# Kernel optimization log

Hardware: AMD Instinct MI355X
Metric: run time of the kernel (lower is better)

Reference implementation:

```python
import jax, jax.numpy as jnp
import numpy as np

EPS = 1e-6


def setup_inputs() -> dict:
    key = jax.random.key(0)
    k = jax.random.split(key, 6)
    B, C_in, C_out, H, W, E = 32, 256, 256, 64, 64, 1024
    x = jax.random.normal(k[0], (B, C_in, H, W), dtype=jnp.float32)
    emb = jax.random.normal(k[1], (B, E), dtype=jnp.float32)
    # adaLN Linear(E -> 2*C_in). (Module zero-inits these; random here for coverage.)
    ada_w = jax.random.normal(k[2], (2 * C_in, E), dtype=jnp.float32) * 0.02
    ada_b = jax.random.normal(k[3], (2 * C_in,), dtype=jnp.float32) * 0.02
    # 1x1 Conv2d(C_in -> C_out) weight (C_out, C_in) and bias
    conv_w = jax.random.normal(k[4], (C_out, C_in), dtype=jnp.float32) * (1.0 / np.sqrt(C_in))
    conv_b = jax.random.normal(k[5], (C_out,), dtype=jnp.float32) * 0.02
    return {"x": x, "emb": emb, "ada_w": ada_w, "ada_b": ada_b,
            "conv_w": conv_w, "conv_b": conv_b}


def reference(x, emb, ada_w, ada_b, conv_w, conv_b):
    # adaLN modulation: SiLU(emb) @ W^T + b -> (B, 2C) -> shift, scale
    mod = jax.nn.silu(emb) @ ada_w.T + ada_b          # (B, 2C)
    shift, scale = jnp.split(mod, 2, axis=1)          # each (B, C)
    # RMSNorm over channel dim (no affine)
    rms = jax.lax.rsqrt(jnp.mean(x * x, axis=1, keepdims=True) + EPS)  # (B,1,H,W)
    xn = x * rms
    # modulate: x * (1 + scale) + shift, broadcast over H,W
    xm = xn * (1.0 + scale[:, :, None, None]) + shift[:, :, None, None]
    # 1x1 conv == channel GEMM
    y = jnp.einsum('bchw,oc->bohw', xm, conv_w) + conv_b[None, :, None, None]
    return jax.nn.selu(y)
```

## Files before the change

### kernel.cpp

```cpp
#include <hip/hip_runtime.h>
#include <hip/hip_bf16.h>

typedef __attribute__((ext_vector_type(4))) float f32x4;
typedef __attribute__((ext_vector_type(8))) short s16x8;
typedef __attribute__((ext_vector_type(4))) unsigned short u16x4;

__device__ __forceinline__ unsigned short f2bf(float f) {
  unsigned u = __builtin_bit_cast(unsigned, f);
  u += 0x7fffu + ((u >> 16) & 1u);
  return (unsigned short)(u >> 16);
}

__global__ __launch_bounds__(512) void k_mod(const float* __restrict__ emb,
                                             const float* __restrict__ ada_w,
                                             const float* __restrict__ ada_b,
                                             float* __restrict__ mod) {
  __shared__ __align__(16) float semb[32][1028];
  const int t = threadIdx.x;
  for (int i = t; i < 8192; i += 512) {
    f32x4 v = ((const f32x4*)emb)[i];
    f32x4 s;
#pragma unroll
    for (int j = 0; j < 4; ++j) s[j] = v[j] / (1.f + __expf(-v[j]));
    *(f32x4*)&semb[i >> 8][(i & 255) << 2] = s;
  }
  __syncthreads();
  const int jl = t >> 5, b = t & 31;
  const int j = blockIdx.x * 16 + jl;
  const f32x4* aw = (const f32x4*)(ada_w + (size_t)j * 1024);
  float acc = 0.f;
  for (int q = 0; q < 256; ++q) {
    f32x4 a = aw[q];
    f32x4 sv = *(const f32x4*)&semb[b][q * 4];
    acc += a[0] * sv[0] + a[1] * sv[1] + a[2] * sv[2] + a[3] * sv[3];
  }
  mod[b * 512 + j] = acc + ada_b[j];
}

__global__ __launch_bounds__(256) void k_prep(const float* __restrict__ mod,
                                              const float* __restrict__ conv_w,
                                              const float* __restrict__ conv_b,
                                              unsigned short* __restrict__ wp,
                                              float* __restrict__ dvec) {
  const int b = blockIdx.y;
  const int o = blockIdx.x * 4 + (threadIdx.x >> 6);
  const int l = threadIdx.x & 63;
  const float* sh = mod + b * 512;
  const float* sc = mod + b * 512 + 256;
  f32x4 cw = ((const f32x4*)(conv_w + (size_t)o * 256))[l];
  f32x4 s4 = ((const f32x4*)sc)[l];
  f32x4 h4 = ((const f32x4*)sh)[l];
  u16x4 wq;
#pragma unroll
  for (int j = 0; j < 4; ++j) wq[j] = f2bf(cw[j] * (1.f + s4[j]));
  const int wr = o >> 6, m = (o >> 4) & 3, lr = o & 15;
  const int kk = l >> 3, g = (l >> 1) & 3, jb = 4 * (l & 1);
  *(u16x4*)(wp + (size_t)b * 65536 + (((wr * 4 + m) * 8 + kk) * 512 + g * 128 + lr * 8 + jb)) = wq;
  float dd = cw[0] * h4[0] + cw[1] * h4[1] + cw[2] * h4[2] + cw[3] * h4[3];
#pragma unroll
  for (int off = 32; off; off >>= 1) dd += __shfl_down(dd, off);
  if (l == 0) dvec[b * 256 + o] = dd + conv_b[o];
}

__global__ __launch_bounds__(512, 2) void k_main(const float* __restrict__ x,
                                                 const unsigned short* __restrict__ wp,
                                                 const float* __restrict__ dvec,
                                                 float* __restrict__ out) {
  constexpr int HW = 4096;
  __shared__ __align__(16) float xf[2][32][256];
  __shared__ float prt[2][256];
  __shared__ float rms[256];

  const int t = threadIdx.x;
  const int b = blockIdx.y;
  const int s0 = blockIdx.x * 256;
  const int w = t >> 6, lane = t & 63;
  const int wr = w >> 1, wc = w & 1;
  const int lr = lane & 15, g = lane >> 4;

  const float* xb = x + (size_t)b * (256 * HW) + s0;
  const unsigned short* A2 = wp + (size_t)b * 65536;

#define ISSUE(K, BUF)                                                                     \
  {                                                                                       \
    _Pragma("unroll") for (int i = 0; i < 4; ++i) {                                       \
      const float* gp = xb + (size_t)((K)*32 + w * 4 + i) * HW + lane * 4;                \
      void* lp = (void*)&xf[BUF][w * 4 + i][0];                                           \
      __builtin_amdgcn_global_load_lds((const __attribute__((address_space(1))) void*)gp, \
                                       (__attribute__((address_space(3))) void*)lp, 16,   \
                                       0, 0);                                             \
    }                                                                                     \
  }

  ISSUE(0, 0);
  ISSUE(1, 1);

  const int sS = t & 255, ch = t >> 8;
  float rs = 0.f;
  f32x4 acc[4][8];
#pragma unroll
  for (int m = 0; m < 4; ++m)
#pragma unroll
    for (int n = 0; n < 8; ++n) acc[m][n] = f32x4{0.f, 0.f, 0.f, 0.f};

#pragma unroll
  for (int k = 0; k < 8; ++k) {
    const int buf = k & 1;
    if (k < 7) {
      asm volatile("s_waitcnt vmcnt(4)" ::: "memory");
    } else {
      asm volatile("s_waitcnt vmcnt(0)" ::: "memory");
    }
    __builtin_amdgcn_s_barrier();

#pragma unroll
    for (int i = 0; i < 16; ++i) {
      float v = xf[buf][ch * 16 + i][sS];
      rs += v * v;
    }

    s16x8 af[4];
#pragma unroll
    for (int m = 0; m < 4; ++m)
      af[m] = *(const s16x8*)(A2 + (((wr * 4 + m) * 8 + k) * 512 + lane * 8));
#pragma unroll
    for (int n = 0; n < 8; ++n) {
      const int s = 128 * wc + 16 * n + lr;
      s16x8 bf;
#pragma unroll
      for (int j = 0; j < 8; ++j) bf[j] = (short)f2bf(xf[buf][g * 8 + j][s]);
#pragma unroll
      for (int m = 0; m < 4; ++m)
        acc[m][n] = __builtin_amdgcn_mfma_f32_16x16x32_bf16(af[m], bf, acc[m][n], 0, 0, 0);
    }

    asm volatile("s_waitcnt lgkmcnt(0)" ::: "memory");
    __builtin_amdgcn_s_barrier();
    if (k < 6) ISSUE(k + 2, buf);
  }
#undef ISSUE

  prt[ch][sS] = rs;
  __syncthreads();
  if (t < 256) rms[t] = rsqrtf((prt[0][t] + prt[1][t]) * (1.0f / 256.0f) + 1e-6f);
  __syncthreads();

  float rr[8];
#pragma unroll
  for (int n = 0; n < 8; ++n) rr[n] = rms[128 * wc + 16 * n + lr];
  float* ob = out + (size_t)b * (256 * HW) + s0;
#pragma unroll
  for (int m = 0; m < 4; ++m) {
    const int o0 = 64 * wr + 16 * m + 4 * g;
    const f32x4 dv = *(const f32x4*)(dvec + (size_t)b * 256 + o0);
#pragma unroll
    for (int n = 0; n < 8; ++n) {
#pragma unroll
      for (int r = 0; r < 4; ++r) {
        float v = rr[n] * acc[m][n][r] + dv[r];
        float res = v > 0.f ? 1.0507009873554805f * v
                            : 1.7580993408473766f * (__expf(v) - 1.f);
        ob[(size_t)(o0 + r) * HW + 128 * wc + 16 * n + lr] = res;
      }
    }
  }
}

extern "C" void kernel_launch(void* const* d_in, const int* in_sizes, int n_in,
                              void* d_out, int out_size, void* d_ws, size_t ws_size,
                              hipStream_t stream) {
  const float* x      = (const float*)d_in[0];
  const float* emb    = (const float*)d_in[1];
  const float* ada_w  = (const float*)d_in[2];
  const float* ada_b  = (const float*)d_in[3];
  const float* conv_w = (const float*)d_in[4];
  const float* conv_b = (const float*)d_in[5];
  float* out = (float*)d_out;

  float* mod  = (float*)d_ws;
  float* dvec = mod + 32 * 512;
  unsigned short* wp = (unsigned short*)(dvec + 32 * 256);

  k_mod<<<dim3(32), 512, 0, stream>>>(emb, ada_w, ada_b, mod);
  k_prep<<<dim3(64, 32), 256, 0, stream>>>(mod, conv_w, conv_b, wp, dvec);
  k_main<<<dim3(16, 32), 512, 0, stream>>>(x, wp, dvec, out);
}
```

Baseline: 102.8 us.

## Convert x tile to bf16 once per block into swizzled LDS buffer

Each k-step now has all threads read the fp32 x tile once with vector loads. They accumulate the sum of squares and write a transposed, XOR-swizzled bf16 copy into a separate LDS region. The MFMA B-fragments are then fetched with a single 16-byte LDS read each. Before, every wave did eight strided scalar reads plus bf16 conversions per fragment, repeated across the four row-waves. The RMS reduction moves to cross-lane shuffles. The cost is an extra barrier per k-step and more LDS (80KB per block), which could limit occupancy.

Result: faster. 98.85 us (-3.9%).

```diff
diff --git a/kernel.cpp b/kernel.cpp
--- a/kernel.cpp
+++ b/kernel.cpp
@@ -67,9 +67,11 @@
                                                  const float* __restrict__ dvec,
                                                  float* __restrict__ out) {
   constexpr int HW = 4096;
-  __shared__ __align__(16) float xf[2][32][256];
-  __shared__ float prt[2][256];
-  __shared__ float rms[256];
+  __shared__ __align__(16) unsigned char smem[81920];
+  float(*xf)[32][256] = (float(*)[32][256])smem;
+  unsigned char* bt = smem + 65536;
+  float* prt = (float*)(smem + 65536);
+  float* rms = (float*)(smem + 65536 + 1024);
 
   const int t = threadIdx.x;
   const int b = blockIdx.y;
@@ -95,8 +97,10 @@
   ISSUE(0, 0);
   ISSUE(1, 1);
 
-  const int sS = t & 255, ch = t >> 8;
-  float rs = 0.f;
+  const int cg = lane >> 3;
+  const int sl = 8 * w + (lane & 7);
+  f32x4 ssq = {0.f, 0.f, 0.f, 0.f};
+
   f32x4 acc[4][8];
 #pragma unroll
   for (int m = 0; m < 4; ++m)
@@ -111,13 +115,23 @@
     } else {
       asm volatile("s_waitcnt vmcnt(0)" ::: "memory");
     }
+    asm volatile("s_waitcnt lgkmcnt(0)" ::: "memory");
     __builtin_amdgcn_s_barrier();
 
-#pragma unroll
-    for (int i = 0; i < 16; ++i) {
-      float v = xf[buf][ch * 16 + i][sS];
-      rs += v * v;
-    }
+    f32x4 vv[4];
+#pragma unroll
+    for (int dc = 0; dc < 4; ++dc) vv[dc] = *(const f32x4*)&xf[buf][4 * cg + dc][4 * sl];
+#pragma unroll
+    for (int dc = 0; dc < 4; ++dc) ssq += vv[dc] * vv[dc];
+#pragma unroll
+    for (int si = 0; si < 4; ++si) {
+      const int s = 4 * sl + si;
+      const int vs = (s >> 4) & 3;
+      u16x4 pk = {f2bf(vv[0][si]), f2bf(vv[1][si]), f2bf(vv[2][si]), f2bf(vv[3][si])};
+      *(u16x4*)(bt + s * 64 + ((cg ^ (2 * vs)) << 3)) = pk;
+    }
+    asm volatile("s_waitcnt lgkmcnt(0)" ::: "memory");
+    __builtin_amdgcn_s_barrier();
 
     s16x8 af[4];
 #pragma unroll
@@ -126,23 +140,26 @@
 #pragma unroll
     for (int n = 0; n < 8; ++n) {
       const int s = 128 * wc + 16 * n + lr;
-      s16x8 bf;
-#pragma unroll
-      for (int j = 0; j < 8; ++j) bf[j] = (short)f2bf(xf[buf][g * 8 + j][s]);
+      const int vs = n & 3;
+      s16x8 bf = *(const s16x8*)(bt + s * 64 + ((g ^ vs) << 4));
 #pragma unroll
       for (int m = 0; m < 4; ++m)
         acc[m][n] = __builtin_amdgcn_mfma_f32_16x16x32_bf16(af[m], bf, acc[m][n], 0, 0, 0);
     }
-
-    asm volatile("s_waitcnt lgkmcnt(0)" ::: "memory");
-    __builtin_amdgcn_s_barrier();
     if (k < 6) ISSUE(k + 2, buf);
   }
 #undef ISSUE
 
-  prt[ch][sS] = rs;
-  __syncthreads();
-  if (t < 256) rms[t] = rsqrtf((prt[0][t] + prt[1][t]) * (1.0f / 256.0f) + 1e-6f);
+  asm volatile("s_waitcnt lgkmcnt(0)" ::: "memory");
+  __syncthreads();
+#pragma unroll
+  for (int off = 8; off <= 32; off <<= 1) {
+#pragma unroll
+    for (int j = 0; j < 4; ++j) ssq[j] += __shfl_xor(ssq[j], off);
+  }
+  if (lane < 8) *(f32x4*)&prt[4 * (8 * w + lane)] = ssq;
+  __syncthreads();
+  if (t < 256) rms[t] = rsqrtf(prt[t] * (1.0f / 256.0f) + 1e-6f);
   __syncthreads();
 
   float rr[8];
```
